# Kernel optimization log

Measured on AMD Instinct MI355X. Metric: run time of the kernel, lower is better.

Reference implementation:

```python
import jax, jax.numpy as jnp
import numpy as np

CURV_BOUNDS = (-2.0, 2.0)
THRESH = 0.01   # |k| below this -> Euclidean branch
EPS = 1e-5

B, S, D = 4, 2048, 512


def setup_inputs() -> dict:
    key = jax.random.key(0)
    ks = jax.random.split(key, 8)
    x = jax.random.normal(ks[0], (B, S, D), jnp.float32)
    sc = 1.0 / np.sqrt(D)  # ~ nn.Linear default init scale
    Wq = jax.random.uniform(ks[1], (D, D), jnp.float32, -sc, sc)
    bq = jax.random.uniform(ks[2], (D,), jnp.float32, -sc, sc)
    Wk = jax.random.uniform(ks[3], (D, D), jnp.float32, -sc, sc)
    bk = jax.random.uniform(ks[4], (D,), jnp.float32, -sc, sc)
    Wv = jax.random.uniform(ks[5], (D, D), jnp.float32, -sc, sc)
    bv = jax.random.uniform(ks[6], (D,), jnp.float32, -sc, sc)
    curvature_raw = jnp.float32(0.5)   # init_curvature
    temperature = jnp.float32(1.0)
    mask = jnp.triu(jnp.ones((S, S), dtype=bool), 1)  # causal: True = masked out
    return {"x": x, "Wq": Wq, "bq": bq, "Wk": Wk, "bk": bk, "Wv": Wv,
            "bv": bv, "curvature_raw": curvature_raw,
            "temperature": temperature, "mask": mask}


def _curvature(raw):
    k_min, k_max = CURV_BOUNDS
    return k_min + (k_max - k_min) * (jnp.tanh(raw) + 1.0) / 2.0


def _project(u, k):
    # project_to_manifold: identity (euclid), Poincare-ball clip (k<0), sphere renorm (k>0)
    n = jnp.sqrt(jnp.sum(u * u, axis=-1, keepdims=True) + 1e-12)
    absk = jnp.abs(k)
    sk = jnp.sqrt(jnp.maximum(absk, EPS))
    max_norm = (1.0 - 1e-3) / sk                      # ball radius 1/sqrt(|k|)
    u_hyp = u * jnp.minimum(1.0, max_norm / n)
    u_sph = u / (n * sk)                              # sphere radius 1/sqrt(k)
    return jnp.where(absk < THRESH, u, jnp.where(k < 0, u_hyp, u_sph))


def reference(x, Wq, bq, Wk, bk, Wv, bv, curvature_raw, temperature, mask):
    k = _curvature(curvature_raw)
    q = x @ Wq.T + bq
    kk = x @ Wk.T + bk
    v = x @ Wv.T + bv
    qm = _project(q, k)
    km = _project(kk, k)

    # pairwise quantities without materializing [B,S,S,D]
    dots = jnp.einsum('bid,bjd->bij', qm, km)         # [B,S,S]
    qn2 = jnp.sum(qm * qm, axis=-1)                   # [B,S]
    kn2 = jnp.sum(km * km, axis=-1)                   # [B,S]
    diff2 = jnp.maximum(qn2[:, :, None] + kn2[:, None, :] - 2.0 * dots, 0.0)

    absk = jnp.abs(k)
    sk = jnp.sqrt(jnp.maximum(absk, EPS))

    d_euc = jnp.sqrt(diff2 + 1e-12)
    # hyperbolic (Poincare ball, c=|k|): acosh(1 + 2c|x-y|^2 / ((1-c|x|^2)(1-c|y|^2))) / sqrt(c)
    denom = jnp.maximum((1.0 - absk * qn2)[:, :, None] * (1.0 - absk * kn2)[:, None, :], EPS)
    arg = 1.0 + 2.0 * absk * diff2 / denom
    d_hyp = jnp.arccosh(jnp.maximum(arg, 1.0 + 1e-7)) / sk
    # spherical (radius 1/sqrt(k)): arccos(k * <x,y>) / sqrt(k)
    cosang = jnp.clip(absk * dots, -1.0 + 1e-7, 1.0 - 1e-7)
    d_sph = jnp.arccos(cosang) / sk

    dist = jnp.where(absk < THRESH, d_euc, jnp.where(k < 0, d_hyp, d_sph))

    scores = -dist / (temperature + 1e-8)
    scores = jnp.where(mask[None, :, :], -jnp.inf, scores)
    attention = jax.nn.softmax(scores, axis=-1)       # [B,S,S]
    output = jnp.einsum('bij,bjd->bid', attention, v) # [B,S,D]
    return output, attention
```

## Files before the change

kernel.cpp:

```cpp
#include <hip/hip_runtime.h>
#include <hip/hip_bf16.h>
#include <math.h>

typedef unsigned short u16;
typedef float float4e __attribute__((ext_vector_type(4)));
typedef short short8 __attribute__((ext_vector_type(8)));
typedef unsigned short ushort8 __attribute__((ext_vector_type(8)));
typedef unsigned short u16x4 __attribute__((ext_vector_type(4)));

#define SEQ 2048
#define DIM 512
#define NB  4

__device__ __forceinline__ float bf2f(u16 h) {
    return __uint_as_float(((unsigned)h) << 16);
}
__device__ __forceinline__ u16 f2bf(float f) {
    __hip_bfloat16 h = __float2bfloat16(f);
    return *reinterpret_cast<u16*>(&h);
}
__device__ __forceinline__ float curv_of(float raw) {
    return -2.0f + 2.0f * (tanhf(raw) + 1.0f);
}
__device__ __forceinline__ void gl_lds16(const u16* g, u16* lds) {
    __builtin_amdgcn_global_load_lds(
        (const __attribute__((address_space(1))) unsigned int*)g,
        (__attribute__((address_space(3))) unsigned int*)lds, 16, 0, 0);
}

__global__ __launch_bounds__(256) void cvt_all_kernel(
    const float* __restrict__ x, const float* __restrict__ Wq,
    const float* __restrict__ Wk, const float* __restrict__ Wv,
    u16* __restrict__ x_bf, u16* __restrict__ Wcat,
    float* __restrict__ lsum, float* __restrict__ qn2r, float* __restrict__ kn2r)
{
    const int n_x = NB * SEQ * DIM, n_w = DIM * DIM;
    int gid = blockIdx.x * 256 + threadIdx.x;
    if (gid < NB * SEQ) { lsum[gid] = 0.f; qn2r[gid] = 0.f; kn2r[gid] = 0.f; }
    int i4 = gid * 4;
    if (i4 < n_x) {
        float4 v = *(const float4*)&x[i4];
        u16x4 h = {f2bf(v.x), f2bf(v.y), f2bf(v.z), f2bf(v.w)};
        *(u16x4*)&x_bf[i4] = h;
    } else if (i4 < n_x + 3 * n_w) {
        int j = i4 - n_x;
        const float* W = (j < n_w) ? Wq : (j < 2 * n_w ? Wk : Wv);
        int off = j % n_w;
        float4 v = *(const float4*)&W[off];
        u16x4 h = {f2bf(v.x), f2bf(v.y), f2bf(v.z), f2bf(v.w)};
        *(u16x4*)&Wcat[j] = h;
    }
}

__global__ __launch_bounds__(256, 2) void gemm_qkv_kernel(
    const u16* __restrict__ A, const u16* __restrict__ Bt,
    u16* __restrict__ qbuf, u16* __restrict__ kbuf, u16* __restrict__ vT,
    const float* __restrict__ bq, const float* __restrict__ bk, const float* __restrict__ bv,
    float* __restrict__ qn2r, float* __restrict__ kn2r)
{
    const int lda = 512, ldb = 512;
    int n = blockIdx.x;
    int xcd = n & 7, i = n >> 3;
    int bn = i % 12, bm = xcd + 8 * (i / 12);

    __shared__ __align__(16) u16 As[128 * 64];
    __shared__ __align__(16) u16 Bs[128 * 64];

    int t = threadIdx.x, wave = t >> 6, lane = t & 63;
    int wr = wave >> 1, wc = wave & 1;
    int lrow = lane & 15, quad = lane >> 4;
    int srow = lane >> 3, sc8 = lane & 7;

    const u16* Ab = A + (size_t)(bm * 128) * lda;
    const u16* Bb = Bt + (size_t)(bn * 128) * ldb;

    float4e acc[4][4];
#pragma unroll
    for (int i2 = 0; i2 < 4; i2++)
#pragma unroll
        for (int j = 0; j < 4; j++) acc[i2][j] = (float4e){0.f, 0.f, 0.f, 0.f};

    for (int kt = 0; kt < 8; ++kt) {
        int k0 = kt << 6;
        __syncthreads();
#pragma unroll
        for (int h = 0; h < 4; ++h) {
            int q = wave * 4 + h;
            int row = q * 8 + srow;
            int c = sc8 ^ (row & 7);
            gl_lds16(Ab + (size_t)row * lda + k0 + c * 8, &As[q * 512]);
            gl_lds16(Bb + (size_t)row * ldb + k0 + c * 8, &Bs[q * 512]);
        }
        __syncthreads();
#pragma unroll
        for (int kk = 0; kk < 2; ++kk) {
            short8 af[4], bfr[4];
#pragma unroll
            for (int im = 0; im < 4; im++) {
                int R = wr * 64 + im * 16 + lrow;
                af[im] = *(const short8*)&As[R * 64 + (((kk * 4 + quad) ^ (R & 7)) * 8)];
            }
#pragma unroll
            for (int in = 0; in < 4; in++) {
                int R = wc * 64 + in * 16 + lrow;
                bfr[in] = *(const short8*)&Bs[R * 64 + (((kk * 4 + quad) ^ (R & 7)) * 8)];
            }
#pragma unroll
            for (int im = 0; im < 4; im++)
#pragma unroll
                for (int in = 0; in < 4; in++)
                    acc[im][in] = __builtin_amdgcn_mfma_f32_16x16x32_bf16(af[im], bfr[in], acc[im][in], 0, 0, 0);
        }
    }

    int region = bn >> 2;
    float nsum[4][4];
#pragma unroll
    for (int im = 0; im < 4; im++)
#pragma unroll
        for (int r = 0; r < 4; r++) nsum[im][r] = 0.f;

#pragma unroll
    for (int in = 0; in < 4; in++) {
        int gj = bn * 128 + wc * 64 + in * 16 + lrow;
        float bias = (gj < 512) ? bq[gj] : (gj < 1024 ? bk[gj - 512] : bv[gj - 1024]);
#pragma unroll
        for (int im = 0; im < 4; im++) {
            int gi0 = bm * 128 + wr * 64 + im * 16 + quad * 4;
            u16x4 pack;
#pragma unroll
            for (int r = 0; r < 4; r++) {
                u16 hv = f2bf(acc[im][in][r] + bias);
                pack[r] = hv;
                if (region == 0) {
                    qbuf[(size_t)(gi0 + r) * 512 + gj] = hv;
                } else if (region == 1) {
                    kbuf[(size_t)(gi0 + r) * 512 + (gj - 512)] = hv;
                }
                if (region < 2) { float vv = bf2f(hv); nsum[im][r] += vv * vv; }
            }
            if (region == 2) {
                int bb = gi0 >> 11, s = gi0 & 2047;
                *(u16x4*)&vT[((size_t)bb * DIM + (gj - 1024)) * SEQ + s] = pack;
            }
        }
    }
    if (region < 2) {
        float* nrm = (region == 0) ? qn2r : kn2r;
#pragma unroll
        for (int im = 0; im < 4; im++)
#pragma unroll
            for (int r = 0; r < 4; r++) {
                float v = nsum[im][r];
                v += __shfl_xor(v, 1);
                v += __shfl_xor(v, 2);
                v += __shfl_xor(v, 4);
                v += __shfl_xor(v, 8);
                if (lrow == 0)
                    atomicAdd(&nrm[bm * 128 + wr * 64 + im * 16 + quad * 4 + r], v);
            }
    }
}

__global__ __launch_bounds__(256) void rownorm_kernel(
    const float* __restrict__ qn2r, const float* __restrict__ kn2r,
    float2* __restrict__ qpk, float2* __restrict__ kpk,
    const float* __restrict__ curvp)
{
    int i = blockIdx.x * 256 + threadIdx.x;
    float kv = curv_of(curvp[0]);
    float absk = fabsf(kv);
    float sk = sqrtf(fmaxf(absk, 1e-5f));
    bool euc = (absk < 0.01f);
    float mxn = (1.0f - 1e-3f) / sk;

    float qr = qn2r[i];
    float nq = sqrtf(qr + 1e-12f);
    float sq_ = euc ? 1.f : (kv < 0.f ? fminf(1.f, mxn / nq) : 1.f / (nq * sk));
    qpk[i] = make_float2(qr * sq_ * sq_, sq_);

    float kr = kn2r[i];
    float nk = sqrtf(kr + 1e-12f);
    float sk_ = euc ? 1.f : (kv < 0.f ? fminf(1.f, mxn / nk) : 1.f / (nk * sk));
    kpk[i] = make_float2(kr * sk_ * sk_, sk_);
}

__global__ __launch_bounds__(512, 4) void gemm_scores_kernel(
    const u16* __restrict__ qbuf, const u16* __restrict__ kbuf,
    u16* __restrict__ attnH, float* __restrict__ lsum,
    const float2* __restrict__ qpk, const float2* __restrict__ kpk,
    const float* __restrict__ curvp, const float* __restrict__ tempp)
{
    const int lda = 512, ldb = 512, ldc = SEQ;
    int n = blockIdx.x;
    int xcd = n & 7, i = n >> 3;
    int bn = i & 15;
    int j = i >> 4;
    int b = j >> 1;
    int bm = (j & 1) ? xcd : 15 - xcd;
    if (bn > bm) return;

    __shared__ __align__(16) u16 As[128 * 64];
    __shared__ __align__(16) u16 Bs[128 * 64];

    int t = threadIdx.x, wave = t >> 6, lane = t & 63;
    int wr = wave >> 2, wc = wave & 3;
    int lrow = lane & 15, quad = lane >> 4;
    int srow = lane >> 3, sc8 = lane & 7;

    const u16* Ab = qbuf + (size_t)(b * SEQ + bm * 128) * lda;
    const u16* Bb = kbuf + (size_t)(b * SEQ + bn * 128) * ldb;

    float4e acc[4][2];
#pragma unroll
    for (int i2 = 0; i2 < 4; i2++)
#pragma unroll
        for (int j2 = 0; j2 < 2; j2++) acc[i2][j2] = (float4e){0.f, 0.f, 0.f, 0.f};

    for (int kt = 0; kt < 8; ++kt) {
        int k0 = kt << 6;
        __syncthreads();
#pragma unroll
        for (int h = 0; h < 2; ++h) {
            int q = wave * 2 + h;
            int row = q * 8 + srow;
            int c = sc8 ^ (row & 7);
            gl_lds16(Ab + (size_t)row * lda + k0 + c * 8, &As[q * 512]);
            gl_lds16(Bb + (size_t)row * ldb + k0 + c * 8, &Bs[q * 512]);
        }
        __syncthreads();
#pragma unroll
        for (int kk = 0; kk < 2; ++kk) {
            short8 af[4], bfr[2];
#pragma unroll
            for (int im = 0; im < 4; im++) {
                int R = wr * 64 + im * 16 + lrow;
                af[im] = *(const short8*)&As[R * 64 + (((kk * 4 + quad) ^ (R & 7)) * 8)];
            }
#pragma unroll
            for (int in = 0; in < 2; in++) {
                int R = wc * 32 + in * 16 + lrow;
                bfr[in] = *(const short8*)&Bs[R * 64 + (((kk * 4 + quad) ^ (R & 7)) * 8)];
            }
#pragma unroll
            for (int im = 0; im < 4; im++)
#pragma unroll
                for (int in = 0; in < 2; in++)
                    acc[im][in] = __builtin_amdgcn_mfma_f32_16x16x32_bf16(af[im], bfr[in], acc[im][in], 0, 0, 0);
        }
    }

    float kv = curv_of(curvp[0]);
    float absk = fabsf(kv);
    float sk = sqrtf(fmaxf(absk, 1e-5f));
    bool euc = (absk < 0.01f);
    float invT = 1.0f / (tempp[0] + 1e-8f);
    float Cexp = -1.4426950408889634f * invT;
    u16* Cb = attnH + (size_t)b * SEQ * SEQ;

    float2 kp[2];
#pragma unroll
    for (int in = 0; in < 2; in++)
        kp[in] = kpk[b * SEQ + bn * 128 + wc * 32 + in * 16 + lrow];

    float psum[4][4];
#pragma unroll
    for (int im = 0; im < 4; im++)
#pragma unroll
        for (int r = 0; r < 4; r++) psum[im][r] = 0.f;

#pragma unroll
    for (int im = 0; im < 4; im++) {
#pragma unroll
        for (int r = 0; r < 4; r++) {
            int gi = bm * 128 + wr * 64 + im * 16 + quad * 4 + r;
            float2 qp = qpk[b * SEQ + gi];
            float qn = qp.x;
#pragma unroll
            for (int in = 0; in < 2; in++) {
                int gj = bn * 128 + wc * 32 + in * 16 + lrow;
                float kn = kp[in].x;
                float dot = acc[im][in][r] * qp.y * kp[in].y;
                float diff2 = fmaxf(qn + kn - 2.f * dot, 0.f);
                float dist;
                if (euc) {
                    dist = sqrtf(diff2 + 1e-12f);
                } else if (kv < 0.f) {
                    float denom = fmaxf((1.f - absk * qn) * (1.f - absk * kn), 1e-5f);
                    float arg = fmaxf(1.f + 2.f * absk * diff2 / denom, 1.f + 1e-7f);
                    dist = acoshf(arg) / sk;
                } else {
                    float c = fminf(fmaxf(absk * dot, -1.f + 1e-7f), 1.f - 1e-7f);
                    dist = acosf(c) / sk;
                }
                float e = (gj <= gi) ? exp2f(dist * Cexp) : 0.f;
                Cb[(size_t)gi * ldc + gj] = f2bf(e);
                psum[im][r] += e;
            }
        }
    }
#pragma unroll
    for (int im = 0; im < 4; im++)
#pragma unroll
        for (int r = 0; r < 4; r++) {
            float v = psum[im][r];
            v += __shfl_xor(v, 1);
            v += __shfl_xor(v, 2);
            v += __shfl_xor(v, 4);
            v += __shfl_xor(v, 8);
            if (lrow == 0) {
                int gi = bm * 128 + wr * 64 + im * 16 + quad * 4 + r;
                atomicAdd(&lsum[b * SEQ + gi], v);
            }
        }
}

__global__ __launch_bounds__(256, 4) void gemm_pv_kernel(
    const u16* __restrict__ attnH, const u16* __restrict__ vT,
    float* __restrict__ out, float* __restrict__ attnF,
    const float* __restrict__ lsum)
{
    const int lda = SEQ, ldb = SEQ, ldc = DIM;
    int n = blockIdx.x;
    int xcd = n & 7, i = n >> 3;
    int bn = i & 7;
    int g = i >> 3;
    int b = g >> 2, q = g & 3;
    int bm = (q == 0) ? xcd : (q == 1) ? 31 - xcd : (q == 2) ? xcd + 8 : 23 - xcd;

    __shared__ __align__(16) u16 As[64 * 64];
    __shared__ __align__(16) u16 Bs[64 * 64];

    int t = threadIdx.x, wave = t >> 6, lane = t & 63;
    int wr = wave >> 1, wc = wave & 1;
    int lrow = lane & 15, quad = lane >> 4;
    int srow = lane >> 3, sc = lane & 7;

    const u16* Ab = attnH + (size_t)b * SEQ * SEQ + (size_t)(bm * 64) * lda;
    const u16* Bb = vT + (size_t)b * DIM * SEQ + (size_t)(bn * 64) * ldb;
    float* attnFb = attnF + (size_t)b * SEQ * SEQ;

    {
        int r = t >> 2, c4 = t & 3;
        float4 z = (float4){0.f, 0.f, 0.f, 0.f};
        for (int kt = bm + 1; kt < 32; ++kt)
            if ((kt & 7) == bn) {
                float* dst = attnFb + (size_t)(bm * 64 + r) * SEQ + kt * 64 + c4 * 16;
                ((float4*)dst)[0] = z; ((float4*)dst)[1] = z;
                ((float4*)dst)[2] = z; ((float4*)dst)[3] = z;
            }
    }

    float4e acc[2][2];
#pragma unroll
    for (int i2 = 0; i2 < 2; i2++)
#pragma unroll
        for (int j2 = 0; j2 < 2; j2++) acc[i2][j2] = (float4e){0.f, 0.f, 0.f, 0.f};

    for (int kt = 0; kt <= bm; ++kt) {
        int k0 = kt << 6;
        __syncthreads();
#pragma unroll
        for (int h = 0; h < 2; ++h) {
            int q2 = wave * 2 + h;
            int row = q2 * 8 + srow;
            int c = sc ^ (row & 7);
            gl_lds16(Ab + (size_t)row * lda + k0 + c * 8, &As[q2 * 512]);
            gl_lds16(Bb + (size_t)row * ldb + k0 + c * 8, &Bs[q2 * 512]);
        }
        __syncthreads();
#pragma unroll
        for (int s = 0; s < 2; ++s) {
            short8 af[2], bfr[2];
#pragma unroll
            for (int im = 0; im < 2; im++) {
                int R = wr * 32 + im * 16 + lrow;
                af[im] = *(const short8*)&As[R * 64 + (((s * 4 + quad) ^ (R & 7)) * 8)];
            }
#pragma unroll
            for (int in = 0; in < 2; in++) {
                int R = wc * 32 + in * 16 + lrow;
                bfr[in] = *(const short8*)&Bs[R * 64 + (((s * 4 + quad) ^ (R & 7)) * 8)];
            }
#pragma unroll
            for (int im = 0; im < 2; im++)
#pragma unroll
                for (int in = 0; in < 2; in++)
                    acc[im][in] = __builtin_amdgcn_mfma_f32_16x16x32_bf16(af[im], bfr[in], acc[im][in], 0, 0, 0);
        }
        if ((kt & 7) == bn) {
            int r = t >> 2, c4 = t & 3;
            int gi = bm * 64 + r;
            float invl = 1.0f / lsum[b * SEQ + gi];
            const u16* src = &As[r * 64];
            int j0 = c4 * 2;
            ushort8 u0 = *(const ushort8*)&src[(j0 ^ (r & 7)) * 8];
            ushort8 u1 = *(const ushort8*)&src[((j0 + 1) ^ (r & 7)) * 8];
            float* dst = attnFb + (size_t)gi * SEQ + kt * 64 + c4 * 16;
            float4 f0 = {bf2f(u0[0]) * invl, bf2f(u0[1]) * invl, bf2f(u0[2]) * invl, bf2f(u0[3]) * invl};
            float4 f1 = {bf2f(u0[4]) * invl, bf2f(u0[5]) * invl, bf2f(u0[6]) * invl, bf2f(u0[7]) * invl};
            float4 f2 = {bf2f(u1[0]) * invl, bf2f(u1[1]) * invl, bf2f(u1[2]) * invl, bf2f(u1[3]) * invl};
            float4 f3 = {bf2f(u1[4]) * invl, bf2f(u1[5]) * invl, bf2f(u1[6]) * invl, bf2f(u1[7]) * invl};
            ((float4*)dst)[0] = f0; ((float4*)dst)[1] = f1;
            ((float4*)dst)[2] = f2; ((float4*)dst)[3] = f3;
        }
    }

    float* Cb = out + (size_t)b * SEQ * DIM;
#pragma unroll
    for (int im = 0; im < 2; im++)
#pragma unroll
        for (int r = 0; r < 4; r++) {
            int gi = bm * 64 + wr * 32 + im * 16 + quad * 4 + r;
            float invl = 1.0f / lsum[b * SEQ + gi];
#pragma unroll
            for (int in = 0; in < 2; in++) {
                int gd = bn * 64 + wc * 32 + in * 16 + lrow;
                Cb[(size_t)gi * ldc + gd] = acc[im][in][r] * invl;
            }
        }
}

extern "C" void kernel_launch(void* const* d_in, const int* in_sizes, int n_in,
                              void* d_out, int out_size, void* d_ws, size_t ws_size,
                              hipStream_t stream) {
    (void)in_sizes; (void)n_in; (void)out_size; (void)ws_size;

    const float* x    = (const float*)d_in[0];
    const float* Wq   = (const float*)d_in[1];
    const float* bq   = (const float*)d_in[2];
    const float* Wk   = (const float*)d_in[3];
    const float* bk   = (const float*)d_in[4];
    const float* Wv   = (const float*)d_in[5];
    const float* bv   = (const float*)d_in[6];
    const float* curv = (const float*)d_in[7];
    const float* temp = (const float*)d_in[8];

    float* out   = (float*)d_out;
    float* attnF = out + (size_t)NB * SEQ * DIM;

    char* ws = (char*)d_ws;
    u16*   x_bf  = (u16*)(ws + 0);
    u16*   Wcat  = (u16*)(ws + 8388608);
    u16*   attnH = (u16*)(ws + 0);
    u16*   qbuf  = (u16*)(ws + 33554432);
    u16*   kbuf  = (u16*)(ws + 41943040);
    u16*   vT    = (u16*)(ws + 50331648);
    float* qn2r  = (float*)(ws + 58720256);
    float* kn2r  = (float*)(ws + 58753024);
    float* lsum  = (float*)(ws + 58785792);
    float2* qpk  = (float2*)(ws + 58818560);
    float2* kpk  = (float2*)(ws + 58884096);

    {
        int n_tot = (NB * SEQ * DIM + 3 * DIM * DIM) / 4;
        cvt_all_kernel<<<(n_tot + 255) / 256, 256, 0, stream>>>(
            x, Wq, Wk, Wv, x_bf, Wcat, lsum, qn2r, kn2r);
    }

    gemm_qkv_kernel<<<768, 256, 0, stream>>>(
        x_bf, Wcat, qbuf, kbuf, vT, bq, bk, bv, qn2r, kn2r);

    rownorm_kernel<<<NB * SEQ / 256, 256, 0, stream>>>(qn2r, kn2r, qpk, kpk, curv);

    gemm_scores_kernel<<<1024, 512, 0, stream>>>(
        qbuf, kbuf, attnH, lsum, qpk, kpk, curv, temp);

    gemm_pv_kernel<<<1024, 256, 0, stream>>>(
        attnH, vT, out, attnF, lsum);
}
```

Before: 227.4 us.

## Use 8-wave blocks with smaller per-wave tiles in QKV and PV GEMMs

Both the QKV projection GEMM and the PV GEMM now run 512-thread blocks of 8 waves, each wave owning a 16-column slice instead of a 2x2 or 4x4 MFMA tile. The QKV GEMM shrinks its N tile from 128 to 64 and doubles the grid to 1536 blocks. This cuts accumulator registers per wave to raise occupancy and latency hiding. In exchange each wave reuses its loaded fragments less (more LDS reads per MFMA), and the QKV kernel reloads the A tile twice as often.

```diff
diff --git a/kernel.cpp b/kernel.cpp
--- a/kernel.cpp
+++ b/kernel.cpp
@@ -52,7 +52,7 @@
     }
 }
 
-__global__ __launch_bounds__(256, 2) void gemm_qkv_kernel(
+__global__ __launch_bounds__(512, 8) void gemm_qkv_kernel(
     const u16* __restrict__ A, const u16* __restrict__ Bt,
     u16* __restrict__ qbuf, u16* __restrict__ kbuf, u16* __restrict__ vT,
     const float* __restrict__ bq, const float* __restrict__ bk, const float* __restrict__ bv,
@@ -61,59 +61,59 @@
     const int lda = 512, ldb = 512;
     int n = blockIdx.x;
     int xcd = n & 7, i = n >> 3;
-    int bn = i % 12, bm = xcd + 8 * (i / 12);
+    int bn = i % 24, bm = xcd + 8 * (i / 24);
 
     __shared__ __align__(16) u16 As[128 * 64];
-    __shared__ __align__(16) u16 Bs[128 * 64];
+    __shared__ __align__(16) u16 Bs[64 * 64];
 
     int t = threadIdx.x, wave = t >> 6, lane = t & 63;
-    int wr = wave >> 1, wc = wave & 1;
+    int wr = wave >> 2, wc = wave & 3;
     int lrow = lane & 15, quad = lane >> 4;
     int srow = lane >> 3, sc8 = lane & 7;
 
     const u16* Ab = A + (size_t)(bm * 128) * lda;
-    const u16* Bb = Bt + (size_t)(bn * 128) * ldb;
-
-    float4e acc[4][4];
-#pragma unroll
-    for (int i2 = 0; i2 < 4; i2++)
-#pragma unroll
-        for (int j = 0; j < 4; j++) acc[i2][j] = (float4e){0.f, 0.f, 0.f, 0.f};
+    const u16* Bb = Bt + (size_t)(bn * 64) * ldb;
+
+    float4e acc[4];
+#pragma unroll
+    for (int i2 = 0; i2 < 4; i2++) acc[i2] = (float4e){0.f, 0.f, 0.f, 0.f};
 
     for (int kt = 0; kt < 8; ++kt) {
         int k0 = kt << 6;
         __syncthreads();
 #pragma unroll
-        for (int h = 0; h < 4; ++h) {
-            int q = wave * 4 + h;
-            int row = q * 8 + srow;
+        for (int h = 0; h < 2; ++h) {
+            int row = h * 64 + wave * 8 + srow;
             int c = sc8 ^ (row & 7);
-            gl_lds16(Ab + (size_t)row * lda + k0 + c * 8, &As[q * 512]);
-            gl_lds16(Bb + (size_t)row * ldb + k0 + c * 8, &Bs[q * 512]);
+            gl_lds16(Ab + (size_t)row * lda + k0 + c * 8, &As[h * 4096 + wave * 512]);
+        }
+        {
+            int row = wave * 8 + srow;
+            int c = sc8 ^ (row & 7);
+            gl_lds16(Bb + (size_t)row * ldb + k0 + c * 8, &Bs[wave * 512]);
         }
         __syncthreads();
 #pragma unroll
         for (int kk = 0; kk < 2; ++kk) {
-            short8 af[4], bfr[4];
+            short8 af[4], bfr;
 #pragma unroll
             for (int im = 0; im < 4; im++) {
                 int R = wr * 64 + im * 16 + lrow;
                 af[im] = *(const short8*)&As[R * 64 + (((kk * 4 + quad) ^ (R & 7)) * 8)];
             }
-#pragma unroll
-            for (int in = 0; in < 4; in++) {
-                int R = wc * 64 + in * 16 + lrow;
-                bfr[in] = *(const short8*)&Bs[R * 64 + (((kk * 4 + quad) ^ (R & 7)) * 8)];
+            {
+                int R = wc * 16 + lrow;
+                bfr = *(const short8*)&Bs[R * 64 + (((kk * 4 + quad) ^ (R & 7)) * 8)];
             }
 #pragma unroll
             for (int im = 0; im < 4; im++)
-#pragma unroll
-                for (int in = 0; in < 4; in++)
-                    acc[im][in] = __builtin_amdgcn_mfma_f32_16x16x32_bf16(af[im], bfr[in], acc[im][in], 0, 0, 0);
-        }
-    }
-
-    int region = bn >> 2;
+                acc[im] = __builtin_amdgcn_mfma_f32_16x16x32_bf16(af[im], bfr, acc[im], 0, 0, 0);
+        }
+    }
+
+    int region = bn >> 3;
+    int gj = bn * 64 + wc * 16 + lrow;
+    float bias = (gj < 512) ? bq[gj] : (gj < 1024 ? bk[gj - 512] : bv[gj - 1024]);
     float nsum[4][4];
 #pragma unroll
     for (int im = 0; im < 4; im++)
@@ -121,28 +121,23 @@
         for (int r = 0; r < 4; r++) nsum[im][r] = 0.f;
 
 #pragma unroll
-    for (int in = 0; in < 4; in++) {
-        int gj = bn * 128 + wc * 64 + in * 16 + lrow;
-        float bias = (gj < 512) ? bq[gj] : (gj < 1024 ? bk[gj - 512] : bv[gj - 1024]);
-#pragma unroll
-        for (int im = 0; im < 4; im++) {
-            int gi0 = bm * 128 + wr * 64 + im * 16 + quad * 4;
-            u16x4 pack;
-#pragma unroll
-            for (int r = 0; r < 4; r++) {
-                u16 hv = f2bf(acc[im][in][r] + bias);
-                pack[r] = hv;
-                if (region == 0) {
-                    qbuf[(size_t)(gi0 + r) * 512 + gj] = hv;
-                } else if (region == 1) {
-                    kbuf[(size_t)(gi0 + r) * 512 + (gj - 512)] = hv;
-                }
-                if (region < 2) { float vv = bf2f(hv); nsum[im][r] += vv * vv; }
-            }
-            if (region == 2) {
-                int bb = gi0 >> 11, s = gi0 & 2047;
-                *(u16x4*)&vT[((size_t)bb * DIM + (gj - 1024)) * SEQ + s] = pack;
-            }
+    for (int im = 0; im < 4; im++) {
+        int gi0 = bm * 128 + wr * 64 + im * 16 + quad * 4;
+        u16x4 pack;
+#pragma unroll
+        for (int r = 0; r < 4; r++) {
+            u16 hv = f2bf(acc[im][r] + bias);
+            pack[r] = hv;
+            if (region == 0) {
+                qbuf[(size_t)(gi0 + r) * 512 + gj] = hv;
+            } else if (region == 1) {
+                kbuf[(size_t)(gi0 + r) * 512 + (gj - 512)] = hv;
+            }
+            if (region < 2) { float vv = bf2f(hv); nsum[im][r] += vv * vv; }
+        }
+        if (region == 2) {
+            int bb = gi0 >> 11, s = gi0 & 2047;
+            *(u16x4*)&vT[((size_t)bb * DIM + (gj - 1024)) * SEQ + s] = pack;
         }
     }
     if (region < 2) {
@@ -315,7 +310,7 @@
         }
 }
 
-__global__ __launch_bounds__(256, 4) void gemm_pv_kernel(
+__global__ __launch_bounds__(512, 8) void gemm_pv_kernel(
     const u16* __restrict__ attnH, const u16* __restrict__ vT,
     float* __restrict__ out, float* __restrict__ attnF,
     const float* __restrict__ lsum)
@@ -332,7 +327,7 @@
     __shared__ __align__(16) u16 Bs[64 * 64];
 
     int t = threadIdx.x, wave = t >> 6, lane = t & 63;
-    int wr = wave >> 1, wc = wave & 1;
+    int wr = wave >> 2, wc = wave & 3;
     int lrow = lane & 15, quad = lane >> 4;
     int srow = lane >> 3, sc = lane & 7;
 
@@ -341,68 +336,55 @@
     float* attnFb = attnF + (size_t)b * SEQ * SEQ;
 
     {
-        int r = t >> 2, c4 = t & 3;
+        int r = t >> 3, c8 = t & 7;
         float4 z = (float4){0.f, 0.f, 0.f, 0.f};
         for (int kt = bm + 1; kt < 32; ++kt)
             if ((kt & 7) == bn) {
-                float* dst = attnFb + (size_t)(bm * 64 + r) * SEQ + kt * 64 + c4 * 16;
+                float* dst = attnFb + (size_t)(bm * 64 + r) * SEQ + kt * 64 + c8 * 8;
                 ((float4*)dst)[0] = z; ((float4*)dst)[1] = z;
-                ((float4*)dst)[2] = z; ((float4*)dst)[3] = z;
-            }
-    }
-
-    float4e acc[2][2];
-#pragma unroll
-    for (int i2 = 0; i2 < 2; i2++)
-#pragma unroll
-        for (int j2 = 0; j2 < 2; j2++) acc[i2][j2] = (float4e){0.f, 0.f, 0.f, 0.f};
+            }
+    }
+
+    float4e acc[2];
+#pragma unroll
+    for (int i2 = 0; i2 < 2; i2++) acc[i2] = (float4e){0.f, 0.f, 0.f, 0.f};
 
     for (int kt = 0; kt <= bm; ++kt) {
         int k0 = kt << 6;
         __syncthreads();
-#pragma unroll
-        for (int h = 0; h < 2; ++h) {
-            int q2 = wave * 2 + h;
-            int row = q2 * 8 + srow;
+        {
+            int row = wave * 8 + srow;
             int c = sc ^ (row & 7);
-            gl_lds16(Ab + (size_t)row * lda + k0 + c * 8, &As[q2 * 512]);
-            gl_lds16(Bb + (size_t)row * ldb + k0 + c * 8, &Bs[q2 * 512]);
+            gl_lds16(Ab + (size_t)row * lda + k0 + c * 8, &As[wave * 512]);
+            gl_lds16(Bb + (size_t)row * ldb + k0 + c * 8, &Bs[wave * 512]);
         }
         __syncthreads();
 #pragma unroll
         for (int s = 0; s < 2; ++s) {
-            short8 af[2], bfr[2];
+            short8 af[2], bfr;
 #pragma unroll
             for (int im = 0; im < 2; im++) {
                 int R = wr * 32 + im * 16 + lrow;
                 af[im] = *(const short8*)&As[R * 64 + (((s * 4 + quad) ^ (R & 7)) * 8)];
             }
-#pragma unroll
-            for (int in = 0; in < 2; in++) {
-                int R = wc * 32 + in * 16 + lrow;
-                bfr[in] = *(const short8*)&Bs[R * 64 + (((s * 4 + quad) ^ (R & 7)) * 8)];
+            {
+                int R = wc * 16 + lrow;
+                bfr = *(const short8*)&Bs[R * 64 + (((s * 4 + quad) ^ (R & 7)) * 8)];
             }
 #pragma unroll
             for (int im = 0; im < 2; im++)
-#pragma unroll
-                for (int in = 0; in < 2; in++)
-                    acc[im][in] = __builtin_amdgcn_mfma_f32_16x16x32_bf16(af[im], bfr[in], acc[im][in], 0, 0, 0);
+                acc[im] = __builtin_amdgcn_mfma_f32_16x16x32_bf16(af[im], bfr, acc[im], 0, 0, 0);
         }
         if ((kt & 7) == bn) {
-            int r = t >> 2, c4 = t & 3;
+            int r = t >> 3, c8 = t & 7;
             int gi = bm * 64 + r;
             float invl = 1.0f / lsum[b * SEQ + gi];
             const u16* src = &As[r * 64];
-            int j0 = c4 * 2;
-            ushort8 u0 = *(const ushort8*)&src[(j0 ^ (r & 7)) * 8];
-            ushort8 u1 = *(const ushort8*)&src[((j0 + 1) ^ (r & 7)) * 8];
-            float* dst = attnFb + (size_t)gi * SEQ + kt * 64 + c4 * 16;
+            ushort8 u0 = *(const ushort8*)&src[(c8 ^ (r & 7)) * 8];
+            float* dst = attnFb + (size_t)gi * SEQ + kt * 64 + c8 * 8;
             float4 f0 = {bf2f(u0[0]) * invl, bf2f(u0[1]) * invl, bf2f(u0[2]) * invl, bf2f(u0[3]) * invl};
             float4 f1 = {bf2f(u0[4]) * invl, bf2f(u0[5]) * invl, bf2f(u0[6]) * invl, bf2f(u0[7]) * invl};
-            float4 f2 = {bf2f(u1[0]) * invl, bf2f(u1[1]) * invl, bf2f(u1[2]) * invl, bf2f(u1[3]) * invl};
-            float4 f3 = {bf2f(u1[4]) * invl, bf2f(u1[5]) * invl, bf2f(u1[6]) * invl, bf2f(u1[7]) * invl};
             ((float4*)dst)[0] = f0; ((float4*)dst)[1] = f1;
-            ((float4*)dst)[2] = f2; ((float4*)dst)[3] = f3;
         }
     }
 
@@ -413,11 +395,8 @@
         for (int r = 0; r < 4; r++) {
             int gi = bm * 64 + wr * 32 + im * 16 + quad * 4 + r;
             float invl = 1.0f / lsum[b * SEQ + gi];
-#pragma unroll
-            for (int in = 0; in < 2; in++) {
-                int gd = bn * 64 + wc * 32 + in * 16 + lrow;
-                Cb[(size_t)gi * ldc + gd] = acc[im][in][r] * invl;
-            }
+            int gd = bn * 64 + wc * 16 + lrow;
+            Cb[(size_t)gi * ldc + gd] = acc[im][r] * invl;
         }
 }
 
@@ -458,7 +437,7 @@
             x, Wq, Wk, Wv, x_bf, Wcat, lsum, qn2r, kn2r);
     }
 
-    gemm_qkv_kernel<<<768, 256, 0, stream>>>(
+    gemm_qkv_kernel<<<1536, 512, 0, stream>>>(
         x_bf, Wcat, qbuf, kbuf, vT, bq, bk, bv, qn2r, kn2r);
 
     rownorm_kernel<<<NB * SEQ / 256, 256, 0, stream>>>(qn2r, kn2r, qpk, kpk, curv);
@@ -466,6 +445,6 @@
     gemm_scores_kernel<<<1024, 512, 0, stream>>>(
         qbuf, kbuf, attnH, lsum, qpk, kpk, curv, temp);
 
-    gemm_pv_kernel<<<1024, 256, 0, stream>>>(
+    gemm_pv_kernel<<<1024, 512, 0, stream>>>(
         attnH, vT, out, attnF, lsum);
 }
```

Result: slower. 238.1 us (+4.7%).
